# Kernel tuning notes

Hardware: AMD Instinct MI355X
Metric: run time of the kernel (lower is better)

## Reference

```python
import jax, jax.numpy as jnp
import numpy as np

NEG_INF = -1.0e9  # matches masked_fill value in the torch module


def setup_inputs() -> dict:
    key = jax.random.key(0)
    ks = jax.random.split(key, 5)
    B, Tx = 32, 1024
    enc_hid, dec_hid, attn = 1024, 1024, 1024
    dec_hidden = jax.random.normal(ks[0], (B, dec_hid), dtype=jnp.float32)
    enc_outputs = jax.random.normal(ks[1], (B, Tx, enc_hid), dtype=jnp.float32)
    mask = jax.random.randint(ks[2], (B, Tx), 0, 2, dtype=jnp.int32)
    # ensure at least one real position per row (avoid all-masked softmax)
    mask = mask.at[:, 0].set(1)
    # nn.Linear params: weight [out, in], bias [out]
    W_w = jax.random.normal(ks[3], (attn, enc_hid + dec_hid), dtype=jnp.float32) * (1.0 / np.sqrt(enc_hid + dec_hid))
    W_b = jnp.zeros((attn,), dtype=jnp.float32)
    v_w = jax.random.normal(ks[4], (1, attn), dtype=jnp.float32) * (1.0 / np.sqrt(attn))
    return {"dec_hidden": dec_hidden, "enc_outputs": enc_outputs, "mask": mask,
            "W_w": W_w, "W_b": W_b, "v_w": v_w}


def reference(dec_hidden, enc_outputs, mask, W_w, W_b, v_w):
    # dec_hidden: [B, D], enc_outputs: [B, Tx, E], mask: [B, Tx]
    B, Tx, E = enc_outputs.shape
    D = dec_hidden.shape[-1]
    # Split W into decoder and encoder halves to avoid materializing the concat:
    # W([h; e]) = h @ W_dec^T + e @ W_enc^T + b
    W_dec = W_w[:, :D]   # [attn, D]
    W_enc = W_w[:, D:]   # [attn, E]
    dec_proj = jnp.einsum('bd,ad->ba', dec_hidden, W_dec)       # [B, attn]
    enc_proj = jnp.einsum('bte,ae->bta', enc_outputs, W_enc)    # [B, Tx, attn]
    energy = jnp.tanh(dec_proj[:, None, :] + enc_proj + W_b)    # [B, Tx, attn]
    scores = jnp.einsum('bta,a->bt', energy, v_w[0])            # [B, Tx]
    scores = jnp.where(mask == 0, NEG_INF, scores)
    alpha = jax.nn.softmax(scores, axis=1)                      # [B, Tx]
    context = jnp.einsum('bt,bte->be', alpha, enc_outputs)      # [B, E]
    return (context, alpha)
```

## Files before the change

kernel.cpp:

```cpp
#include <hip/hip_runtime.h>
#include <hip/hip_bf16.h>

typedef __bf16 bf16_t;
typedef __bf16 bf16x8_t __attribute__((ext_vector_type(8)));
typedef float f32x4_t __attribute__((ext_vector_type(4)));

#define NEG_BIG -1000000000.0f

__device__ __forceinline__ void gld_lds16(const void* g, void* l) {
    __builtin_amdgcn_global_load_lds((const __attribute__((address_space(1))) void*)g,
                                     (__attribute__((address_space(3))) void*)l,
                                     16, 0, 0);
}

__device__ __forceinline__ float tanh_fast(float x) {
    float e = __expf(2.0f * x);
    return 1.0f - 2.0f / (e + 1.0f);
}

__global__ void k_prep(const float* __restrict__ Ww, const float* __restrict__ dec,
                       const float* __restrict__ Wb, bf16_t* __restrict__ Bw,
                       float* __restrict__ bias, float* __restrict__ score) {
    const int bi = blockIdx.x;
    const int t = threadIdx.x;
    if (bi < 512) {
        size_t flat = (size_t)bi * 2048 + t * 8;
        int a = (int)(flat >> 10), e = (int)(flat & 1023);
        const float* src = Ww + (size_t)a * 2048 + 1024 + e;
        float4 f0 = *(const float4*)src;
        float4 f1 = *(const float4*)(src + 4);
        bf16x8_t v;
        v[0] = (bf16_t)f0.x; v[1] = (bf16_t)f0.y; v[2] = (bf16_t)f0.z; v[3] = (bf16_t)f0.w;
        v[4] = (bf16_t)f1.x; v[5] = (bf16_t)f1.y; v[6] = (bf16_t)f1.z; v[7] = (bf16_t)f1.w;
        *(bf16x8_t*)(Bw + flat) = v;
    } else if (bi < 1536) {
        __shared__ float wrow[1024];
        int a = bi - 512;
        *(float4*)(wrow + t * 4) = *(const float4*)(Ww + (size_t)a * 2048 + t * 4);
        __syncthreads();
        int b = t >> 3, j = t & 7;
        const float* dp = dec + b * 1024 + j * 128;
        const float* wp = wrow + j * 128;
        float s = 0.0f;
#pragma unroll 8
        for (int i = 0; i < 128; i += 4) {
            float4 dv = *(const float4*)(dp + i);
            float4 wv = *(const float4*)(wp + i);
            s += dv.x * wv.x + dv.y * wv.y + dv.z * wv.z + dv.w * wv.w;
        }
        s += __shfl_xor(s, 1);
        s += __shfl_xor(s, 2);
        s += __shfl_xor(s, 4);
        if (j == 0) bias[b * 1024 + a] = s + Wb[a];
    } else {
        float4 z = {0.f, 0.f, 0.f, 0.f};
        *(float4*)(score + (size_t)(bi - 1536) * 1024 + t * 4) = z;
    }
}

__global__ __launch_bounds__(256, 4) void k_gemm_score(
    const float* __restrict__ enc, const bf16_t* __restrict__ Bw,
    const float* __restrict__ bias, const float* __restrict__ v,
    float* __restrict__ scores) {
    __shared__ __attribute__((aligned(16))) bf16_t As[128 * 32];
    __shared__ __attribute__((aligned(16))) bf16_t Bs[128 * 32];

    const int tid = threadIdx.x;
    const int lane = tid & 63;
    const int wid = tid >> 6;
    const int wm = wid >> 1, wn = wid & 1;
    const int lin = blockIdx.x;
    const int bm = (lin & 7) + ((lin >> 6) << 3);
    const int bn = (lin >> 3) & 7;
    const int rsel = lane & 15, kg = lane >> 4;

    f32x4_t acc[4][4] = {};

    const int ar = tid >> 2;
    const int aq = tid & 3;
    const int asw = (tid >> 3) & 3;
    const size_t arow0 = (size_t)(bm * 128 + ar) * 1024;
    const size_t arow1 = (size_t)(bm * 128 + 64 + ar) * 1024;

    const int c0 = wid * 2;
    const int bj = (lane & 3) ^ ((lane >> 3) & 3);
    const bf16_t* bsrc0 = Bw + (size_t)(bn * 128 + c0 * 16 + (lane >> 2)) * 1024 + bj * 8;
    const bf16_t* bsrc1 = bsrc0 + (size_t)16 * 1024;

    for (int kt = 0; kt < 32; ++kt) {
        const int k0 = kt * 32;
        gld_lds16(bsrc0 + k0, Bs + c0 * 512);
        gld_lds16(bsrc1 + k0, Bs + (c0 + 1) * 512);
        {
            const float* s0 = enc + arow0 + k0 + aq * 8;
            float4 f0 = *(const float4*)s0;
            float4 f1 = *(const float4*)(s0 + 4);
            bf16x8_t val;
            val[0] = (bf16_t)f0.x; val[1] = (bf16_t)f0.y; val[2] = (bf16_t)f0.z; val[3] = (bf16_t)f0.w;
            val[4] = (bf16_t)f1.x; val[5] = (bf16_t)f1.y; val[6] = (bf16_t)f1.z; val[7] = (bf16_t)f1.w;
            *(bf16x8_t*)(As + ar * 32 + (aq ^ asw) * 8) = val;
            const float* s1 = enc + arow1 + k0 + aq * 8;
            float4 g0 = *(const float4*)s1;
            float4 g1 = *(const float4*)(s1 + 4);
            bf16x8_t val2;
            val2[0] = (bf16_t)g0.x; val2[1] = (bf16_t)g0.y; val2[2] = (bf16_t)g0.z; val2[3] = (bf16_t)g0.w;
            val2[4] = (bf16_t)g1.x; val2[5] = (bf16_t)g1.y; val2[6] = (bf16_t)g1.z; val2[7] = (bf16_t)g1.w;
            *(bf16x8_t*)(As + (64 + ar) * 32 + (aq ^ asw) * 8) = val2;
        }
        __syncthreads();
        bf16x8_t af[4], bf[4];
        const int ksw = (kg ^ ((rsel >> 1) & 3)) * 8;
#pragma unroll
        for (int fm = 0; fm < 4; ++fm)
            af[fm] = *(const bf16x8_t*)(As + (wm * 64 + fm * 16 + rsel) * 32 + ksw);
#pragma unroll
        for (int fn = 0; fn < 4; ++fn)
            bf[fn] = *(const bf16x8_t*)(Bs + (wn * 64 + fn * 16 + rsel) * 32 + ksw);
#pragma unroll
        for (int fm = 0; fm < 4; ++fm)
#pragma unroll
            for (int fn = 0; fn < 4; ++fn)
                acc[fm][fn] = __builtin_amdgcn_mfma_f32_16x16x32_bf16(af[fm], bf[fn], acc[fm][fn], 0, 0, 0);
        __syncthreads();
    }

    const int b = bm >> 3;
    float bias_l[4], v_l[4];
#pragma unroll
    for (int fn = 0; fn < 4; ++fn) {
        int a = bn * 128 + wn * 64 + fn * 16 + rsel;
        bias_l[fn] = bias[b * 1024 + a];
        v_l[fn] = v[a];
    }
    float part[16];
#pragma unroll
    for (int fm = 0; fm < 4; ++fm)
#pragma unroll
        for (int r = 0; r < 4; ++r) {
            float p = 0.0f;
#pragma unroll
            for (int fn = 0; fn < 4; ++fn) {
                float x = acc[fm][fn][r] + bias_l[fn];
                p += tanh_fast(x) * v_l[fn];
            }
            part[fm * 4 + r] = p;
        }
#pragma unroll
    for (int k = 0; k < 16; ++k) {
        part[k] += __shfl_xor(part[k], 1);
        part[k] += __shfl_xor(part[k], 2);
        part[k] += __shfl_xor(part[k], 4);
        part[k] += __shfl_xor(part[k], 8);
    }
    const int mrow0 = bm * 128 + wm * 64 + kg * 4;
#pragma unroll
    for (int k = 0; k < 16; ++k) {
        if (rsel == k) {
            int fm = k >> 2, r = k & 3;
            atomicAdd(&scores[mrow0 + fm * 16 + r], part[k]);
        }
    }
}

__global__ void k_ctx(const float* __restrict__ enc, const float* __restrict__ scores,
                      const int* __restrict__ mask, float* __restrict__ alpha_out,
                      float* __restrict__ part) {
    __shared__ float red[4];
    __shared__ float red2[4];
    __shared__ float sal[1024];
    const int chunk = blockIdx.x;
    const int b = blockIdx.y;
    const int t = threadIdx.x;

    float4 s = *(const float4*)(scores + b * 1024 + t * 4);
    int4 m = *(const int4*)(mask + b * 1024 + t * 4);
    float v0 = m.x ? s.x : NEG_BIG;
    float v1 = m.y ? s.y : NEG_BIG;
    float v2 = m.z ? s.z : NEG_BIG;
    float v3 = m.w ? s.w : NEG_BIG;
    float mx = fmaxf(fmaxf(v0, v1), fmaxf(v2, v3));
#pragma unroll
    for (int o = 1; o < 64; o <<= 1) mx = fmaxf(mx, __shfl_xor(mx, o));
    if ((t & 63) == 0) red[t >> 6] = mx;
    __syncthreads();
    mx = fmaxf(fmaxf(red[0], red[1]), fmaxf(red[2], red[3]));
    float e0 = m.x ? __expf(v0 - mx) : 0.0f;
    float e1 = m.y ? __expf(v1 - mx) : 0.0f;
    float e2 = m.z ? __expf(v2 - mx) : 0.0f;
    float e3 = m.w ? __expf(v3 - mx) : 0.0f;
    float sum = e0 + e1 + e2 + e3;
#pragma unroll
    for (int o = 1; o < 64; o <<= 1) sum += __shfl_xor(sum, o);
    if ((t & 63) == 0) red2[t >> 6] = sum;
    __syncthreads();
    float inv = 1.0f / (red2[0] + red2[1] + red2[2] + red2[3]);
    float4 al = {e0 * inv, e1 * inv, e2 * inv, e3 * inv};
    *(float4*)(sal + t * 4) = al;
    if (t >= chunk * 8 && t < chunk * 8 + 8)
        *(float4*)(alpha_out + b * 1024 + t * 4) = al;
    __syncthreads();

    const int e = t * 4;
    const float* ep = enc + ((size_t)b * 1024 + chunk * 32) * 1024 + e;
    const float* ap = sal + chunk * 32;
    float ax = 0.f, ay = 0.f, az = 0.f, aw = 0.f;
#pragma unroll 4
    for (int i = 0; i < 32; ++i) {
        float a = ap[i];
        float4 x = *(const float4*)(ep + (size_t)i * 1024);
        ax += a * x.x; ay += a * x.y; az += a * x.z; aw += a * x.w;
    }
    float4 o = {ax, ay, az, aw};
    *(float4*)(part + ((size_t)chunk * 32 + b) * 1024 + e) = o;
}

__global__ void k_ctx_reduce(const float* __restrict__ part, float* __restrict__ ctx) {
    int b = blockIdx.x, t = threadIdx.x;
    int e = t * 4;
    float ax = 0.f, ay = 0.f, az = 0.f, aw = 0.f;
#pragma unroll 8
    for (int c = 0; c < 32; ++c) {
        float4 x = *(const float4*)(part + ((size_t)c * 32 + b) * 1024 + e);
        ax += x.x; ay += x.y; az += x.z; aw += x.w;
    }
    float4 o = {ax, ay, az, aw};
    *(float4*)(ctx + b * 1024 + e) = o;
}

extern "C" void kernel_launch(void* const* d_in, const int* in_sizes, int n_in,
                              void* d_out, int out_size, void* d_ws, size_t ws_size,
                              hipStream_t stream) {
    const float* dec  = (const float*)d_in[0];
    const float* enc  = (const float*)d_in[1];
    const int*   mask = (const int*)d_in[2];
    const float* Ww   = (const float*)d_in[3];
    const float* Wb   = (const float*)d_in[4];
    const float* vw   = (const float*)d_in[5];
    float* out = (float*)d_out;

    char* ws = (char*)d_ws;
    bf16_t* Bw    = (bf16_t*)ws;
    float*  bias  = (float*)(ws + 2097152);
    float*  score = (float*)(ws + 2228224);
    float*  part  = (float*)(ws + 2359296);

    k_prep<<<1568, 256, 0, stream>>>(Ww, dec, Wb, Bw, bias, score);
    k_gemm_score<<<2048, 256, 0, stream>>>(enc, Bw, bias, vw, score);
    k_ctx<<<dim3(32, 32), 256, 0, stream>>>(enc, score, mask, out + 32768, part);
    k_ctx_reduce<<<32, 256, 0, stream>>>(part, out);
}
```

Before: 337.1 us.

## Load GEMM fragments directly from global memory, bypassing LDS staging

The score GEMM no longer stages A and B tiles through shared memory with barriers. Each wave now loads its MFMA fragments straight from global memory (fp32 enc converted to bf16 in registers), and the launch bound is lowered to 3 blocks per SM. This removes LDS traffic and the two block syncs per k-step. In exchange, tiles shared between waves are loaded redundantly (each A row twice, each B row twice), and accesses are strided 16-byte loads per row, which may raise cache pressure and memory latency.

Measured after the change: 550.8 us. 63.4% more time.

```diff
diff --git a/kernel.cpp b/kernel.cpp
--- a/kernel.cpp
+++ b/kernel.cpp
@@ -6,12 +6,6 @@
 typedef float f32x4_t __attribute__((ext_vector_type(4)));
 
 #define NEG_BIG -1000000000.0f
-
-__device__ __forceinline__ void gld_lds16(const void* g, void* l) {
-    __builtin_amdgcn_global_load_lds((const __attribute__((address_space(1))) void*)g,
-                                     (__attribute__((address_space(3))) void*)l,
-                                     16, 0, 0);
-}
 
 __device__ __forceinline__ float tanh_fast(float x) {
     float e = __expf(2.0f * x);
@@ -58,13 +52,10 @@
     }
 }
 
-__global__ __launch_bounds__(256, 4) void k_gemm_score(
+__global__ __launch_bounds__(256, 3) void k_gemm_score(
     const float* __restrict__ enc, const bf16_t* __restrict__ Bw,
     const float* __restrict__ bias, const float* __restrict__ v,
     float* __restrict__ scores) {
-    __shared__ __attribute__((aligned(16))) bf16_t As[128 * 32];
-    __shared__ __attribute__((aligned(16))) bf16_t Bs[128 * 32];
-
     const int tid = threadIdx.x;
     const int lane = tid & 63;
     const int wid = tid >> 6;
@@ -76,52 +67,33 @@
 
     f32x4_t acc[4][4] = {};
 
-    const int ar = tid >> 2;
-    const int aq = tid & 3;
-    const int asw = (tid >> 3) & 3;
-    const size_t arow0 = (size_t)(bm * 128 + ar) * 1024;
-    const size_t arow1 = (size_t)(bm * 128 + 64 + ar) * 1024;
-
-    const int c0 = wid * 2;
-    const int bj = (lane & 3) ^ ((lane >> 3) & 3);
-    const bf16_t* bsrc0 = Bw + (size_t)(bn * 128 + c0 * 16 + (lane >> 2)) * 1024 + bj * 8;
-    const bf16_t* bsrc1 = bsrc0 + (size_t)16 * 1024;
+    const float*  ap = enc + (size_t)(bm * 128 + wm * 64 + rsel) * 1024 + kg * 8;
+    const bf16_t* bp = Bw  + (size_t)(bn * 128 + wn * 64 + rsel) * 1024 + kg * 8;
 
     for (int kt = 0; kt < 32; ++kt) {
         const int k0 = kt * 32;
-        gld_lds16(bsrc0 + k0, Bs + c0 * 512);
-        gld_lds16(bsrc1 + k0, Bs + (c0 + 1) * 512);
-        {
-            const float* s0 = enc + arow0 + k0 + aq * 8;
-            float4 f0 = *(const float4*)s0;
-            float4 f1 = *(const float4*)(s0 + 4);
-            bf16x8_t val;
-            val[0] = (bf16_t)f0.x; val[1] = (bf16_t)f0.y; val[2] = (bf16_t)f0.z; val[3] = (bf16_t)f0.w;
-            val[4] = (bf16_t)f1.x; val[5] = (bf16_t)f1.y; val[6] = (bf16_t)f1.z; val[7] = (bf16_t)f1.w;
-            *(bf16x8_t*)(As + ar * 32 + (aq ^ asw) * 8) = val;
-            const float* s1 = enc + arow1 + k0 + aq * 8;
-            float4 g0 = *(const float4*)s1;
-            float4 g1 = *(const float4*)(s1 + 4);
-            bf16x8_t val2;
-            val2[0] = (bf16_t)g0.x; val2[1] = (bf16_t)g0.y; val2[2] = (bf16_t)g0.z; val2[3] = (bf16_t)g0.w;
-            val2[4] = (bf16_t)g1.x; val2[5] = (bf16_t)g1.y; val2[6] = (bf16_t)g1.z; val2[7] = (bf16_t)g1.w;
-            *(bf16x8_t*)(As + (64 + ar) * 32 + (aq ^ asw) * 8) = val2;
-        }
-        __syncthreads();
-        bf16x8_t af[4], bf[4];
-        const int ksw = (kg ^ ((rsel >> 1) & 3)) * 8;
-#pragma unroll
-        for (int fm = 0; fm < 4; ++fm)
-            af[fm] = *(const bf16x8_t*)(As + (wm * 64 + fm * 16 + rsel) * 32 + ksw);
+        bf16x8_t bf[4];
 #pragma unroll
         for (int fn = 0; fn < 4; ++fn)
-            bf[fn] = *(const bf16x8_t*)(Bs + (wn * 64 + fn * 16 + rsel) * 32 + ksw);
-#pragma unroll
-        for (int fm = 0; fm < 4; ++fm)
+            bf[fn] = *(const bf16x8_t*)(bp + fn * 16 * 1024 + k0);
+        float4 a0[4], a1[4];
+#pragma unroll
+        for (int fm = 0; fm < 4; ++fm) {
+            const float* s = ap + fm * 16 * 1024 + k0;
+            a0[fm] = *(const float4*)s;
+            a1[fm] = *(const float4*)(s + 4);
+        }
+#pragma unroll
+        for (int fm = 0; fm < 4; ++fm) {
+            bf16x8_t af;
+            af[0] = (bf16_t)a0[fm].x; af[1] = (bf16_t)a0[fm].y;
+            af[2] = (bf16_t)a0[fm].z; af[3] = (bf16_t)a0[fm].w;
+            af[4] = (bf16_t)a1[fm].x; af[5] = (bf16_t)a1[fm].y;
+            af[6] = (bf16_t)a1[fm].z; af[7] = (bf16_t)a1[fm].w;
 #pragma unroll
             for (int fn = 0; fn < 4; ++fn)
-                acc[fm][fn] = __builtin_amdgcn_mfma_f32_16x16x32_bf16(af[fm], bf[fn], acc[fm][fn], 0, 0, 0);
-        __syncthreads();
+                acc[fm][fn] = __builtin_amdgcn_mfma_f32_16x16x32_bf16(af, bf[fn], acc[fm][fn], 0, 0, 0);
+        }
     }
 
     const int b = bm >> 3;
```
